# Kernel tuning notes

Measured on AMD Instinct MI355X. Metric: run time of the kernel, lower is better.

The kernel has to match this reference:

```python
import jax, jax.numpy as jnp
import numpy as np

BINS = 10
MMT = 0.9
N = 33554432  # 2^25 elements


def setup_inputs() -> dict:
    key = jax.random.key(0)
    k1, k2, k3 = jax.random.split(key, 3)
    pred = jax.random.normal(k1, (N,), dtype=jnp.float32)
    target = jax.random.randint(k2, (N,), 0, 2, dtype=jnp.int32)
    acc_sum = jax.random.uniform(k3, (BINS,), dtype=jnp.float32)
    return {"pred": pred, "target": target, "acc_sum": acc_sum}


def reference(pred, target, acc_sum):
    bins = acc_sum.shape[0]
    # border = arange(bins+1)/bins, with last edge nudged up by 1e-6
    border = jnp.arange(bins + 1, dtype=jnp.float32) / bins
    border = border.at[-1].add(1e-6)

    t = target.astype(jnp.float32)
    # gradient density measure on detached predictions
    g = jnp.abs(jax.nn.sigmoid(jax.lax.stop_gradient(pred)) - t)
    # bin index: g in [border[i], border[i+1])  ->  i
    idx = jnp.clip(jnp.searchsorted(border, g, side='right') - 1, 0, bins - 1)

    # single-pass histogram (replaces the per-bin mask loop)
    counts = jax.ops.segment_sum(jnp.ones_like(g), idx, num_segments=bins)
    nonempty = counts > 0

    # momentum-accumulated bin statistics (only updated for non-empty bins)
    acc_new = jnp.where(nonempty, MMT * acc_sum + (1.0 - MMT) * counts, acc_sum)

    tot = jnp.float32(max(pred.shape[0], 1.0))
    safe_acc = jnp.where(nonempty, acc_new, 1.0)
    bin_w = jnp.where(nonempty, tot / safe_acc, 0.0)  # [bins]

    n = jnp.sum(nonempty.astype(jnp.float32))
    bin_w = jnp.where(n > 0, bin_w / jnp.maximum(n, 1.0), bin_w)

    # per-element GHM weights are constants w.r.t. pred (buffer + detached g)
    w = jax.lax.stop_gradient(bin_w[idx])

    # BCE-with-logits, numerically stable
    bce = jnp.maximum(pred, 0.0) - pred * t + jnp.log1p(jnp.exp(-jnp.abs(pred)))
    return jnp.sum(w * bce) / tot
```

## Files before the change

kernel.cpp:

```cpp
#include <hip/hip_runtime.h>

#define BINS 10
#define NTHREADS 256


__device__ __forceinline__ float wave_reduce_add(float v) {
#pragma unroll
    for (int off = 32; off > 0; off >>= 1) v += __shfl_down(v, off, 64);
    return v;
}

__global__ __launch_bounds__(NTHREADS) void ghm_pass1(
    const float* __restrict__ pred, const int* __restrict__ target,
    float* __restrict__ g_T,
    unsigned int* __restrict__ g_C,
    int n4, int n)
{
    const float C[BINS] = {0.f,
        2.19722458f, 1.38629436f, 0.84729786f, 0.40546511f, 0.0f,
        -0.40546511f, -0.84729786f, -1.38629436f, -2.19722458f};

    float T[BINS];
    unsigned int cnt[BINS];
#pragma unroll
    for (int b = 0; b < BINS; ++b) { T[b] = 0.f; cnt[b] = 0u; }

    const float4* __restrict__ p4 = reinterpret_cast<const float4*>(pred);
    const int4*   __restrict__ t4 = reinterpret_cast<const int4*>(target);

    const int tid    = threadIdx.x;
    const int gtid   = blockIdx.x * blockDim.x + tid;
    const int stride = gridDim.x * blockDim.x;

    for (int i = gtid; i < n4; i += stride) {
        const float4 xv = p4[i];
        const int4   tv = t4[i];
        const float xs[4] = {xv.x, xv.y, xv.z, xv.w};
        const int   ts[4] = {tv.x, tv.y, tv.z, tv.w};
        cnt[0] += (unsigned int)(4 * __popcll(__ballot(1)));
#pragma unroll
        for (int j = 0; j < 4; ++j) {
            const float x = xs[j];
            const float y = (ts[j] != 0) ? x : -x;
            const float E = __expf(-y);
            const float bce = __logf(1.0f + E);
            T[0] += bce;
#pragma unroll
            for (int b = 1; b < BINS; ++b) {
                const bool p = (y <= C[b]);
                T[b] += p ? bce : 0.0f;
                cnt[b] += (unsigned int)__popcll(__ballot(p));
            }
        }
    }

    if (gtid == 0) {
        for (int i = n4 * 4; i < n; ++i) {
            const float x = pred[i];
            const float y = (target[i] != 0) ? x : -x;
            const float E = __expf(-y);
            const float bce = __logf(1.0f + E);
            T[0] += bce;
            cnt[0] += (unsigned int)__popcll(__ballot(1));
#pragma unroll
            for (int b = 1; b < BINS; ++b) {
                const bool p = (y <= C[b]);
                T[b] += p ? bce : 0.0f;
                cnt[b] += (unsigned int)__popcll(__ballot(p));
            }
        }
    }

    __shared__ float        r_T[BINS];
    __shared__ unsigned int r_C[BINS];
    if (tid < BINS) { r_T[tid] = 0.f; r_C[tid] = 0u; }
    __syncthreads();

    const int lane = tid & 63;
#pragma unroll
    for (int b = 0; b < BINS; ++b) {
        const float v = wave_reduce_add(T[b]);
        if (lane == 0) {
            atomicAdd(&r_T[b], v);
            atomicAdd(&r_C[b], cnt[b]);
        }
    }
    __syncthreads();

    if (tid < BINS) {
        atomicAdd(&g_T[tid], r_T[tid]);
        atomicAdd(&g_C[tid], r_C[tid]);
    }
}

__global__ void ghm_finalize(const float* __restrict__ g_T,
                             const unsigned int* __restrict__ g_C,
                             const float* __restrict__ acc_sum,
                             float* __restrict__ out, float tot)
{
    if (threadIdx.x == 0 && blockIdx.x == 0) {
        float S[BINS];
        float cntf[BINS];
#pragma unroll
        for (int b = 0; b < BINS; ++b) {
            const float Tn = (b + 1 < BINS) ? g_T[b + 1] : 0.f;
            const unsigned int Cn = (b + 1 < BINS) ? g_C[b + 1] : 0u;
            S[b]    = g_T[b] - Tn;
            cntf[b] = (float)(g_C[b] - Cn);
        }
        float binw[BINS];
        int nne = 0;
#pragma unroll
        for (int b = 0; b < BINS; ++b) {
            const bool ne = (cntf[b] > 0.0f);
            const float accn = ne ? (0.9f * acc_sum[b] + 0.1f * cntf[b]) : acc_sum[b];
            binw[b] = ne ? (tot / accn) : 0.0f;
            nne += ne ? 1 : 0;
        }
        const float scale = (nne > 0) ? (1.0f / (float)nne) : 1.0f;
        float res = 0.0f;
#pragma unroll
        for (int b = 0; b < BINS; ++b) res += (binw[b] * scale) * S[b];
        out[0] = res / tot;
    }
}

extern "C" void kernel_launch(void* const* d_in, const int* in_sizes, int n_in,
                              void* d_out, int out_size, void* d_ws, size_t ws_size,
                              hipStream_t stream) {
    const float* pred    = (const float*)d_in[0];
    const int*   target  = (const int*)d_in[1];
    const float* acc_sum = (const float*)d_in[2];
    float*       out     = (float*)d_out;

    const int n  = in_sizes[0];
    const int n4 = n / 4;

    float*        g_T = (float*)d_ws;
    unsigned int* g_C = (unsigned int*)((float*)d_ws + BINS);

    hipMemsetAsync(d_ws, 0, 2 * BINS * sizeof(float), stream);

    ghm_pass1<<<2048, NTHREADS, 0, stream>>>(pred, target, g_T, g_C, n4, n);

    const float tot = (float)(n > 1 ? n : 1);
    ghm_finalize<<<1, 64, 0, stream>>>(g_T, g_C, acc_sum, out, tot);
}
```

Baseline: 91.77 us.

## Software-pipeline loads, use per-lane counters and native exp2/log2 in GHM pass

```diff
diff --git a/kernel.cpp b/kernel.cpp
--- a/kernel.cpp
+++ b/kernel.cpp
@@ -9,17 +9,29 @@
     for (int off = 32; off > 0; off >>= 1) v += __shfl_down(v, off, 64);
     return v;
 }
+__device__ __forceinline__ unsigned int wave_reduce_addu(unsigned int v) {
+#pragma unroll
+    for (int off = 32; off > 0; off >>= 1) v += __shfl_down((int)v, off, 64);
+    return v;
+}
 
-__global__ __launch_bounds__(NTHREADS) void ghm_pass1(
+#define GHM_C1  2.19722458f
+#define GHM_C2  1.38629436f
+#define GHM_C3  0.84729786f
+#define GHM_C4  0.40546511f
+#define GHM_C5  0.0f
+#define GHM_C6 -0.40546511f
+#define GHM_C7 -0.84729786f
+#define GHM_C8 -1.38629436f
+#define GHM_C9 -2.19722458f
+#define LOG2E 1.44269504f
+
+__global__ __launch_bounds__(NTHREADS, 8) void ghm_pass1(
     const float* __restrict__ pred, const int* __restrict__ target,
     float* __restrict__ g_T,
     unsigned int* __restrict__ g_C,
     int n4, int n)
 {
-    const float C[BINS] = {0.f,
-        2.19722458f, 1.38629436f, 0.84729786f, 0.40546511f, 0.0f,
-        -0.40546511f, -0.84729786f, -1.38629436f, -2.19722458f};
-
     float T[BINS];
     unsigned int cnt[BINS];
 #pragma unroll
@@ -29,47 +41,77 @@
     const int4*   __restrict__ t4 = reinterpret_cast<const int4*>(target);
 
     const int tid    = threadIdx.x;
-    const int gtid   = blockIdx.x * blockDim.x + tid;
-    const int stride = gridDim.x * blockDim.x;
+    const int gtid   = blockIdx.x * NTHREADS + tid;
+    const int stride = gridDim.x * NTHREADS;
+    const int step   = 2 * stride;
 
-    for (int i = gtid; i < n4; i += stride) {
+#define GHM_BODY(xv, tv)                                                     \
+    {                                                                        \
+        const float xs_[4] = {(xv).x, (xv).y, (xv).z, (xv).w};               \
+        const int   ts_[4] = {(tv).x, (tv).y, (tv).z, (tv).w};               \
+        _Pragma("unroll")                                                    \
+        for (int j = 0; j < 4; ++j) {                                        \
+            const float x = xs_[j];                                          \
+            const float y = (ts_[j] != 0) ? x : -x;                          \
+            const float E = __builtin_amdgcn_exp2f(-y * LOG2E);              \
+            const float bce2 = __builtin_amdgcn_logf(1.0f + E);              \
+            T[0] += bce2;                                                    \
+            { const bool p = (y <= GHM_C1); T[1]+=p?bce2:0.f; cnt[1]+=p; }   \
+            { const bool p = (y <= GHM_C2); T[2]+=p?bce2:0.f; cnt[2]+=p; }   \
+            { const bool p = (y <= GHM_C3); T[3]+=p?bce2:0.f; cnt[3]+=p; }   \
+            { const bool p = (y <= GHM_C4); T[4]+=p?bce2:0.f; cnt[4]+=p; }   \
+            { const bool p = (y <= GHM_C5); T[5]+=p?bce2:0.f; cnt[5]+=p; }   \
+            { const bool p = (y <= GHM_C6); T[6]+=p?bce2:0.f; cnt[6]+=p; }   \
+            { const bool p = (y <= GHM_C7); T[7]+=p?bce2:0.f; cnt[7]+=p; }   \
+            { const bool p = (y <= GHM_C8); T[8]+=p?bce2:0.f; cnt[8]+=p; }   \
+            { const bool p = (y <= GHM_C9); T[9]+=p?bce2:0.f; cnt[9]+=p; }   \
+        }                                                                    \
+    }
+
+    const int R = (step > 0) ? (n4 / step) : 0;
+    if (R > 0) {
+        int idx = gtid;
+        float4 xa0 = p4[idx];
+        int4   ta0 = t4[idx];
+        float4 xa1 = p4[idx + stride];
+        int4   ta1 = t4[idx + stride];
+        for (int r = 1; r < R; ++r) {
+            const int nidx = gtid + r * step;
+            const float4 xb0 = p4[nidx];
+            const int4   tb0 = t4[nidx];
+            const float4 xb1 = p4[nidx + stride];
+            const int4   tb1 = t4[nidx + stride];
+            GHM_BODY(xa0, ta0);
+            GHM_BODY(xa1, ta1);
+            xa0 = xb0; ta0 = tb0; xa1 = xb1; ta1 = tb1;
+        }
+        GHM_BODY(xa0, ta0);
+        GHM_BODY(xa1, ta1);
+    }
+    for (int i = gtid + R * step; i < n4; i += stride) {
         const float4 xv = p4[i];
         const int4   tv = t4[i];
-        const float xs[4] = {xv.x, xv.y, xv.z, xv.w};
-        const int   ts[4] = {tv.x, tv.y, tv.z, tv.w};
-        cnt[0] += (unsigned int)(4 * __popcll(__ballot(1)));
-#pragma unroll
-        for (int j = 0; j < 4; ++j) {
-            const float x = xs[j];
-            const float y = (ts[j] != 0) ? x : -x;
-            const float E = __expf(-y);
-            const float bce = __logf(1.0f + E);
-            T[0] += bce;
-#pragma unroll
-            for (int b = 1; b < BINS; ++b) {
-                const bool p = (y <= C[b]);
-                T[b] += p ? bce : 0.0f;
-                cnt[b] += (unsigned int)__popcll(__ballot(p));
-            }
-        }
+        GHM_BODY(xv, tv);
     }
-
     if (gtid == 0) {
         for (int i = n4 * 4; i < n; ++i) {
             const float x = pred[i];
             const float y = (target[i] != 0) ? x : -x;
-            const float E = __expf(-y);
-            const float bce = __logf(1.0f + E);
-            T[0] += bce;
-            cnt[0] += (unsigned int)__popcll(__ballot(1));
-#pragma unroll
-            for (int b = 1; b < BINS; ++b) {
-                const bool p = (y <= C[b]);
-                T[b] += p ? bce : 0.0f;
-                cnt[b] += (unsigned int)__popcll(__ballot(p));
-            }
+            const float E = __builtin_amdgcn_exp2f(-y * LOG2E);
+            const float bce2 = __builtin_amdgcn_logf(1.0f + E);
+            T[0] += bce2;
+            { const bool p = (y <= GHM_C1); T[1]+=p?bce2:0.f; cnt[1]+=p; }
+            { const bool p = (y <= GHM_C2); T[2]+=p?bce2:0.f; cnt[2]+=p; }
+            { const bool p = (y <= GHM_C3); T[3]+=p?bce2:0.f; cnt[3]+=p; }
+            { const bool p = (y <= GHM_C4); T[4]+=p?bce2:0.f; cnt[4]+=p; }
+            { const bool p = (y <= GHM_C5); T[5]+=p?bce2:0.f; cnt[5]+=p; }
+            { const bool p = (y <= GHM_C6); T[6]+=p?bce2:0.f; cnt[6]+=p; }
+            { const bool p = (y <= GHM_C7); T[7]+=p?bce2:0.f; cnt[7]+=p; }
+            { const bool p = (y <= GHM_C8); T[8]+=p?bce2:0.f; cnt[8]+=p; }
+            { const bool p = (y <= GHM_C9); T[9]+=p?bce2:0.f; cnt[9]+=p; }
         }
     }
+#undef GHM_BODY
 
     __shared__ float        r_T[BINS];
     __shared__ unsigned int r_C[BINS];
@@ -79,10 +121,11 @@
     const int lane = tid & 63;
 #pragma unroll
     for (int b = 0; b < BINS; ++b) {
-        const float v = wave_reduce_add(T[b]);
+        const float        v = wave_reduce_add(T[b]);
+        const unsigned int c = (b > 0) ? wave_reduce_addu(cnt[b]) : 0u;
         if (lane == 0) {
             atomicAdd(&r_T[b], v);
-            atomicAdd(&r_C[b], cnt[b]);
+            if (b > 0) atomicAdd(&r_C[b], c);
         }
     }
     __syncthreads();
@@ -96,17 +139,20 @@
 __global__ void ghm_finalize(const float* __restrict__ g_T,
                              const unsigned int* __restrict__ g_C,
                              const float* __restrict__ acc_sum,
-                             float* __restrict__ out, float tot)
+                             float* __restrict__ out, float tot, unsigned int ntot)
 {
     if (threadIdx.x == 0 && blockIdx.x == 0) {
+        const float LN2 = 0.69314718056f;
         float S[BINS];
         float cntf[BINS];
 #pragma unroll
         for (int b = 0; b < BINS; ++b) {
-            const float Tn = (b + 1 < BINS) ? g_T[b + 1] : 0.f;
+            const float        Tc = g_T[b];
+            const float        Tn = (b + 1 < BINS) ? g_T[b + 1] : 0.f;
+            const unsigned int Cc = (b == 0) ? ntot : g_C[b];
             const unsigned int Cn = (b + 1 < BINS) ? g_C[b + 1] : 0u;
-            S[b]    = g_T[b] - Tn;
-            cntf[b] = (float)(g_C[b] - Cn);
+            S[b]    = (Tc - Tn) * LN2;
+            cntf[b] = (float)(Cc - Cn);
         }
         float binw[BINS];
         int nne = 0;
@@ -144,5 +190,5 @@
     ghm_pass1<<<2048, NTHREADS, 0, stream>>>(pred, target, g_T, g_C, n4, n);
 
     const float tot = (float)(n > 1 ? n : 1);
-    ghm_finalize<<<1, 64, 0, stream>>>(g_T, g_C, acc_sum, out, tot);
+    ghm_finalize<<<1, 64, 0, stream>>>(g_T, g_C, acc_sum, out, tot, (unsigned int)n);
 }
```

Measured after the change: 88.55 us. 3.5% less time.
